# Performance work log

Hardware: AMD Instinct MI355X
Metric: run time of the kernel (lower is better)

Reference implementation:

```python
import jax, jax.numpy as jnp
import numpy as np

DIM = 1024
NEXP = 8
TOPK = 2
B, S = 2, 2048
HID = 4 * DIM

# ---- BitLinear (kyegomez/BitNet, 1.58-bit) helpers ----

def rmsnorm(x):
    # SimpleRMSNorm: x / rms(x), no learned scale
    return x * jax.lax.rsqrt(jnp.mean(x * x, axis=-1, keepdims=True) + 1e-6)

def act_quant(x):
    # per-token int8 absmax quant
    scale = 127.0 / jnp.clip(jnp.max(jnp.abs(x), axis=-1, keepdims=True), 1e-5, None)
    return jnp.clip(jnp.round(x * scale), -128, 127) / scale

def weight_quant(w):
    # ternary weight quant with per-tensor mean-abs scale
    scale = 1.0 / jnp.clip(jnp.mean(jnp.abs(w)), 1e-5, None)
    return jnp.clip(jnp.round(w * scale), -1, 1) / scale

def ste(a, q):
    # straight-through estimator: forward q, backward identity on a
    return a + jax.lax.stop_gradient(q - a)

def bit_input(x):
    xn = rmsnorm(x)
    return ste(xn, act_quant(xn))

def bit_weight(w):
    return ste(w, weight_quant(w))


def setup_inputs() -> dict:
    key = jax.random.key(0)
    ks = jax.random.split(key, 6)
    x = jax.random.normal(ks[0], (B, S, DIM), dtype=jnp.float32)
    eps = jax.random.normal(ks[1], (B, S, NEXP), dtype=jnp.float32)
    w_route = jax.random.normal(ks[2], (NEXP, DIM), dtype=jnp.float32) * 0.02
    w_noise = jax.random.normal(ks[3], (NEXP, DIM), dtype=jnp.float32) * 0.02
    w1 = jax.random.normal(ks[4], (NEXP, HID, DIM), dtype=jnp.float32) * 0.02
    w2 = jax.random.normal(ks[5], (NEXP, DIM, HID), dtype=jnp.float32) * 0.02
    return {"x": x, "eps": eps, "w_route": w_route, "w_noise": w_noise, "w1": w1, "w2": w2}


def reference(x, eps, w_route, w_noise, w1, w2):
    Bb, Ss, D = x.shape
    # router: both BitLinears share the same rmsnorm+quant of x (no bias)
    xq = bit_input(x)                                  # [B,S,D]
    logits = xq @ bit_weight(w_route).T                # [B,S,E]
    noise_logits = xq @ bit_weight(w_noise).T          # [B,S,E]
    noisy = logits + eps * jax.nn.softplus(noise_logits)
    _, topi = jax.lax.top_k(noisy, TOPK)               # indices [B,S,K]
    sel = jnp.any(jax.nn.one_hot(topi, NEXP, dtype=jnp.bool_), axis=-2)  # [B,S,E]
    sparse = jnp.where(sel, noisy, -jnp.inf)
    gates = jax.nn.softmax(sparse, axis=-1)            # zeros at unselected experts

    T = Bb * Ss
    xf = xq.reshape(T, D)                              # expert layer-1 input quant == router's
    gf = gates.reshape(T, NEXP)
    w1q = jax.vmap(bit_weight)(w1)                     # [E,H,D]
    w2q = jax.vmap(bit_weight)(w2)                     # [E,D,H]
    h = jax.nn.relu(jnp.einsum('td,ehd->teh', xf, w1q))
    hq = bit_input(h)                                  # per-(token,expert) quant
    y = jnp.einsum('teh,edh->ted', hq, w2q)            # expert outputs
    # gated combine; gates are exactly 0 for unselected experts -> identical to masked scatter-add
    out = jnp.einsum('ted,te->td', y, gf)
    return out.reshape(Bb, Ss, D)
```

## Files before the change

### kernel.cpp

```cpp
#include <hip/hip_runtime.h>
#include <hip/hip_bf16.h>

#define DIMD 1024
#define NEXP 8
#define NTOK 4096
#define HIDN 4096
#define CAP  4096
#define EXPSTRIDE 4194304L

typedef __bf16 bf16;
typedef bf16  bf16x8 __attribute__((ext_vector_type(8)));
typedef float f32x4  __attribute__((ext_vector_type(4)));
typedef int   i32x4  __attribute__((ext_vector_type(4)));
typedef signed char i8x8 __attribute__((ext_vector_type(8)));
typedef signed char i8x4 __attribute__((ext_vector_type(4)));
typedef signed char i8;

__device__ __forceinline__ void gload16(const void* g, void* l) {
  __builtin_amdgcn_global_load_lds(
      (const __attribute__((address_space(1))) unsigned int*)g,
      (__attribute__((address_space(3))) unsigned int*)l, 16, 0, 0);
}

#define VMCNT4 asm volatile("s_waitcnt vmcnt(4)" ::: "memory")
#define VMCNT0 asm volatile("s_waitcnt vmcnt(0)" ::: "memory")
#define BAR    asm volatile("s_barrier" ::: "memory")

__global__ void k_wsum(const float* __restrict__ w1, const float* __restrict__ w2,
                       float* __restrict__ partials) {
  const int slot = blockIdx.y;
  const int b = blockIdx.x;
  const int tid = threadIdx.x;
  const float* src = (slot < 8) ? (w1 + (long)slot * EXPSTRIDE)
                                : (w2 + (long)(slot - 8) * EXPSTRIDE);
  const f32x4* p = (const f32x4*)src;
  float s = 0.f;
  #pragma unroll
  for (int j = 0; j < 32; ++j) {
    f32x4 v = p[(long)b * 8192 + j * 256 + tid];
    s += fabsf(v.x) + fabsf(v.y) + fabsf(v.z) + fabsf(v.w);
  }
  #pragma unroll
  for (int o = 1; o < 64; o <<= 1) s += __shfl_xor(s, o, 64);
  __shared__ float red[4];
  if ((tid & 63) == 0) red[tid >> 6] = s;
  __syncthreads();
  if (tid == 0) partials[slot * 128 + b] = red[0] + red[1] + red[2] + red[3];
}

__global__ void k_finalize(const float* __restrict__ partials,
                           const float* __restrict__ wr, const float* __restrict__ wn,
                           float* __restrict__ wmean,
                           bf16* __restrict__ wrq, bf16* __restrict__ wnq) {
  const int tid = threadIdx.x;
  if (tid < 16) {
    float s = 0.f;
    for (int j = 0; j < 128; ++j) s += partials[tid * 128 + j];
    wmean[tid] = fmaxf(s * (1.0f / 4194304.0f), 1e-5f);
  }
  float sr = 0.f, sn = 0.f;
  #pragma unroll
  for (int j = 0; j < 32; ++j) {
    sr += fabsf(wr[j * 256 + tid]);
    sn += fabsf(wn[j * 256 + tid]);
  }
  #pragma unroll
  for (int o = 1; o < 64; o <<= 1) {
    sr += __shfl_xor(sr, o, 64);
    sn += __shfl_xor(sn, o, 64);
  }
  __shared__ float red[8];
  if ((tid & 63) == 0) { red[tid >> 6] = sr; red[4 + (tid >> 6)] = sn; }
  __syncthreads();
  if (tid == 0) {
    wmean[16] = fmaxf((red[0] + red[1] + red[2] + red[3]) * (1.0f / 8192.0f), 1e-5f);
    wmean[17] = fmaxf((red[4] + red[5] + red[6] + red[7]) * (1.0f / 8192.0f), 1e-5f);
  }
  __syncthreads();
  const float ir = 1.0f / wmean[16];
  const float in = 1.0f / wmean[17];
  for (int j = 0; j < 32; ++j) {
    int i = j * 256 + tid;
    wrq[i] = (bf16)fminf(fmaxf(rintf(wr[i] * ir), -1.f), 1.f);
    wnq[i] = (bf16)fminf(fmaxf(rintf(wn[i] * in), -1.f), 1.f);
  }
}

__global__ void k_wquant(const float* __restrict__ w1, const float* __restrict__ w2,
                         const float* __restrict__ wmean,
                         i8* __restrict__ w1q, i8* __restrict__ w2q) {
  const int tid = threadIdx.x;
  const int which = blockIdx.x >> 14;
  const long lg = (long)(blockIdx.x & 16383) * 256 + tid;
  const int e = (int)(lg >> 19);
  const float inv = 1.0f / wmean[(which ? 8 : 0) + e];
  const float* src = which ? w2 : w1;
  i8* dst = which ? w2q : w1q;
  const f32x4* p = (const f32x4*)src + lg * 2;
  f32x4 v0 = p[0], v1 = p[1];
  i8x8 q;
  q[0] = (i8)fminf(fmaxf(rintf(v0.x * inv), -1.f), 1.f);
  q[1] = (i8)fminf(fmaxf(rintf(v0.y * inv), -1.f), 1.f);
  q[2] = (i8)fminf(fmaxf(rintf(v0.z * inv), -1.f), 1.f);
  q[3] = (i8)fminf(fmaxf(rintf(v0.w * inv), -1.f), 1.f);
  q[4] = (i8)fminf(fmaxf(rintf(v1.x * inv), -1.f), 1.f);
  q[5] = (i8)fminf(fmaxf(rintf(v1.y * inv), -1.f), 1.f);
  q[6] = (i8)fminf(fmaxf(rintf(v1.z * inv), -1.f), 1.f);
  q[7] = (i8)fminf(fmaxf(rintf(v1.w * inv), -1.f), 1.f);
  *(i8x8*)(dst + lg * 8) = q;
}

__global__ void k_xquant(const float* __restrict__ x, i8* __restrict__ xq,
                         float* __restrict__ sx) {
  const int t = blockIdx.x, tid = threadIdx.x;
  f32x4 v = ((const f32x4*)(x + (long)t * DIMD))[tid];
  float ss = v.x * v.x + v.y * v.y + v.z * v.z + v.w * v.w;
  float am = fmaxf(fmaxf(fabsf(v.x), fabsf(v.y)), fmaxf(fabsf(v.z), fabsf(v.w)));
  #pragma unroll
  for (int o = 1; o < 64; o <<= 1) {
    ss += __shfl_xor(ss, o, 64);
    am = fmaxf(am, __shfl_xor(am, o, 64));
  }
  __shared__ float red[8];
  if ((tid & 63) == 0) { red[tid >> 6] = ss; red[4 + (tid >> 6)] = am; }
  __syncthreads();
  ss = red[0] + red[1] + red[2] + red[3];
  am = fmaxf(fmaxf(red[4], red[5]), fmaxf(red[6], red[7]));
  const float r = 1.0f / sqrtf(ss * (1.0f / DIMD) + 1e-6f);
  const float amn = fmaxf(am * r, 1e-5f);
  const float s = 127.0f / amn;
  i8x4 q;
  q[0] = (i8)fminf(fmaxf(rintf((v.x * r) * s), -128.f), 127.f);
  q[1] = (i8)fminf(fmaxf(rintf((v.y * r) * s), -128.f), 127.f);
  q[2] = (i8)fminf(fmaxf(rintf((v.z * r) * s), -128.f), 127.f);
  q[3] = (i8)fminf(fmaxf(rintf((v.w * r) * s), -128.f), 127.f);
  *(i8x4*)(xq + (long)t * DIMD + tid * 4) = q;
  if (tid == 0) sx[t] = amn * (1.0f / 127.0f);
}

__global__ void k_router(const i8* __restrict__ xq, const float* __restrict__ sx,
                         const bf16* __restrict__ wrq, const bf16* __restrict__ wnq,
                         const float* __restrict__ eps, const float* __restrict__ wmean,
                         int* __restrict__ cnt, int* __restrict__ idx,
                         float* __restrict__ gate) {
  __shared__ float xf[DIMD];
  __shared__ float dots[16];
  const int t = blockIdx.x, tid = threadIdx.x;
  const i8* xr = xq + (long)t * DIMD;
  #pragma unroll
  for (int j = 0; j < 4; ++j) xf[tid * 4 + j] = (float)xr[tid * 4 + j];
  __syncthreads();
  const int grp = tid >> 4, l16 = tid & 15;
  const bf16* wv = (grp < 8) ? (wrq + grp * DIMD) : (wnq + (grp - 8) * DIMD);
  float s = 0.f;
  #pragma unroll
  for (int j = 0; j < 64; ++j) s += xf[l16 + j * 16] * (float)wv[l16 + j * 16];
  s += __shfl_xor(s, 1, 64); s += __shfl_xor(s, 2, 64);
  s += __shfl_xor(s, 4, 64); s += __shfl_xor(s, 8, 64);
  if (l16 == 0) dots[grp] = s;
  __syncthreads();
  if (tid == 0) {
    const float st = sx[t];
    const float fr = st * wmean[16], fn = st * wmean[17];
    float ny[8];
    #pragma unroll
    for (int e = 0; e < 8; ++e) {
      const float nl = dots[8 + e] * fn;
      const float sp = fmaxf(nl, 0.f) + log1pf(expf(-fabsf(nl)));
      ny[e] = dots[e] * fr + eps[t * 8 + e] * sp;
    }
    int i1 = 0;
    #pragma unroll
    for (int e = 1; e < 8; ++e) if (ny[e] > ny[i1]) i1 = e;
    int i2 = (i1 == 0) ? 1 : 0;
    #pragma unroll
    for (int e = 0; e < 8; ++e) if (e != i1 && ny[e] > ny[i2]) i2 = e;
    const float ex = expf(ny[i2] - ny[i1]);
    const float g1 = 1.0f / (1.0f + ex);
    const float g2 = ex * g1;
    int p1 = atomicAdd(&cnt[i1], 1);
    idx[i1 * CAP + p1] = t; gate[i1 * CAP + p1] = g1;
    int p2 = atomicAdd(&cnt[i2], 1);
    idx[i2 * CAP + p2] = t; gate[i2 * CAP + p2] = g2;
  }
}

__global__ void k_offsets(const int* __restrict__ cnt, int* __restrict__ offs) {
  if (threadIdx.x == 0) {
    int a = 0;
    for (int e = 0; e < NEXP; ++e) { offs[e] = a; a += cnt[e]; }
    offs[8] = a;
  }
}

template <int KD, int LOGNT, bool L1>
__global__ __launch_bounds__(256, 4) void k_gemm(
    const i8* __restrict__ Abase, const i8* __restrict__ Wq,
    const int* __restrict__ cnt, const int* __restrict__ offs,
    const int* __restrict__ idx, const float* __restrict__ gate,
    const float* __restrict__ srow, const float* __restrict__ wmean,
    float* __restrict__ Out) {
  const int bid = blockIdx.x;
  const int xcd = bid & 7;
  const int s = bid >> 3;
  const int pl = s >> 5;
  const int mt = s & 31;
  const int pidx = pl * 8 + xcd;
  const int e = pidx >> LOGNT;
  const int nt = pidx & ((1 << LOGNT) - 1);

  const int c = cnt[e];
  if (mt * 128 >= c) return;
  const int oe = offs[e];
  __shared__ __align__(16) char lds[33280];
  char* lA0 = lds;
  char* lB0 = lds + 8192;
  char* lA1 = lds + 16384;
  char* lB1 = lds + 24576;
  int* tokL = (int*)(lds + 32768);
  const int tid = threadIdx.x, w = tid >> 6, lam = tid & 63;
  if (tid < 128) {
    int i = mt * 128 + tid;
    tokL[tid] = idx[e * CAP + (i < c ? i : c - 1)];
  }
  __syncthreads();

  const i8* aS[2];
  const i8* bS[2];
  #pragma unroll
  for (int i = 0; i < 2; ++i) {
    const int cid = w * 64 + lam + 256 * i;
    const int r = cid >> 2, q = cid & 3;
    const int cg = q ^ ((r >> 1) & 3);
    long arow;
    if (L1) arow = (long)tokL[r];
    else { int ii = mt * 128 + r; arow = (long)oe + (ii < c ? ii : c - 1); }
    aS[i] = Abase + arow * KD + cg * 16;
    bS[i] = Wq + (long)e * EXPSTRIDE + (long)(nt * 128 + r) * KD + cg * 16;
  }
  const int dbase = (w * 64 + lam) * 16;

  auto STAGE = [&](int kb, char* dA, char* dB) {
    #pragma unroll
    for (int i = 0; i < 2; ++i) gload16(aS[i] + kb * 64, dA + dbase + i * 4096);
    #pragma unroll
    for (int i = 0; i < 2; ++i) gload16(bS[i] + kb * 64, dB + dbase + i * 4096);
  };

  const int wr = w >> 1, wc = w & 1;
  int offA[4], offB[4];
  const int cc = lam >> 4;
  #pragma unroll
  for (int m = 0; m < 4; ++m) {
    const int ra = wr * 64 + m * 16 + (lam & 15);
    const int rb = wc * 64 + m * 16 + (lam & 15);
    offA[m] = ra * 64 + ((cc ^ ((ra >> 1) & 3)) << 4);
    offB[m] = rb * 64 + ((cc ^ ((rb >> 1) & 3)) << 4);
  }
  i32x4 acc[4][4];
  #pragma unroll
  for (int m = 0; m < 4; ++m)
    #pragma unroll
    for (int n = 0; n < 4; ++n) acc[m][n] = (i32x4){0, 0, 0, 0};

  auto COMPUTE = [&](const char* cA, const char* cB) {
    i32x4 af[4], bfr[4];
    #pragma unroll
    for (int m = 0; m < 4; ++m) af[m] = *(const i32x4*)(cA + offA[m]);
    #pragma unroll
    for (int n = 0; n < 4; ++n) bfr[n] = *(const i32x4*)(cB + offB[n]);
    #pragma unroll
    for (int m = 0; m < 4; ++m)
      #pragma unroll
      for (int n = 0; n < 4; ++n)
        acc[m][n] = __builtin_amdgcn_mfma_i32_16x16x64_i8(af[m], bfr[n], acc[m][n], 0, 0, 0);
  };

  constexpr int KT = KD / 64;
  STAGE(0, lA0, lB0);
  for (int kb = 0; kb < KT; kb += 2) {
    STAGE(kb + 1, lA1, lB1);
    VMCNT4;
    BAR;
    COMPUTE(lA0, lB0);
    BAR;
    if (kb + 2 < KT) { STAGE(kb + 2, lA0, lB0); VMCNT4; } else { VMCNT0; }
    BAR;
    COMPUTE(lA1, lB1);
    BAR;
  }

  const float wm = wmean[(L1 ? 0 : 8) + e];
  #pragma unroll
  for (int m = 0; m < 4; ++m) {
    #pragma unroll
    for (int r = 0; r < 4; ++r) {
      const int rl = wr * 64 + m * 16 + ((lam >> 4) << 2) + r;
      const int i = mt * 128 + rl;
      if (i < c) {
        if (L1) {
          const float fac = srow[tokL[rl]] * wm;
          float* hp = Out + (long)(oe + i) * HIDN + nt * 128 + wc * 64 + (lam & 15);
          #pragma unroll
          for (int n = 0; n < 4; ++n) hp[n * 16] = fmaxf((float)acc[m][n][r] * fac, 0.f);
        } else {
          const float fac = srow[oe + i] * wm * gate[e * CAP + i];
          float* op = Out + (long)tokL[rl] * DIMD + nt * 128 + wc * 64 + (lam & 15);
          #pragma unroll
          for (int n = 0; n < 4; ++n) atomicAdd(op + n * 16, (float)acc[m][n][r] * fac);
        }
      }
    }
  }
}

__global__ void k_hquant(const float* __restrict__ h, i8* __restrict__ hq,
                         float* __restrict__ sh, const int* __restrict__ offs) {
  const int row = blockIdx.x;
  if (row >= offs[8]) return;
  const int tid = threadIdx.x;
  const f32x4* hr = (const f32x4*)(h + (long)row * HIDN);
  f32x4 v[4];
  float ss = 0.f, am = 0.f;
  #pragma unroll
  for (int j = 0; j < 4; ++j) {
    v[j] = hr[tid + j * 256];
    ss += v[j].x * v[j].x + v[j].y * v[j].y + v[j].z * v[j].z + v[j].w * v[j].w;
    am = fmaxf(am, fmaxf(fmaxf(fabsf(v[j].x), fabsf(v[j].y)),
                         fmaxf(fabsf(v[j].z), fabsf(v[j].w))));
  }
  #pragma unroll
  for (int o = 1; o < 64; o <<= 1) {
    ss += __shfl_xor(ss, o, 64);
    am = fmaxf(am, __shfl_xor(am, o, 64));
  }
  __shared__ float red[8];
  if ((tid & 63) == 0) { red[tid >> 6] = ss; red[4 + (tid >> 6)] = am; }
  __syncthreads();
  ss = red[0] + red[1] + red[2] + red[3];
  am = fmaxf(fmaxf(red[4], red[5]), fmaxf(red[6], red[7]));
  const float r = 1.0f / sqrtf(ss * (1.0f / HIDN) + 1e-6f);
  const float amn = fmaxf(am * r, 1e-5f);
  const float s = 127.0f / amn;
  i8* dst = hq + (long)row * HIDN;
  #pragma unroll
  for (int j = 0; j < 4; ++j) {
    i8x4 q;
    q[0] = (i8)fminf(fmaxf(rintf((v[j].x * r) * s), -128.f), 127.f);
    q[1] = (i8)fminf(fmaxf(rintf((v[j].y * r) * s), -128.f), 127.f);
    q[2] = (i8)fminf(fmaxf(rintf((v[j].z * r) * s), -128.f), 127.f);
    q[3] = (i8)fminf(fmaxf(rintf((v[j].w * r) * s), -128.f), 127.f);
    *(i8x4*)(dst + (tid + j * 256) * 4) = q;
  }
  if (tid == 0) sh[row] = amn * (1.0f / 127.0f);
}

extern "C" void kernel_launch(void* const* d_in, const int* in_sizes, int n_in,
                              void* d_out, int out_size, void* d_ws, size_t ws_size,
                              hipStream_t stream) {
  const float* x   = (const float*)d_in[0];
  const float* eps = (const float*)d_in[1];
  const float* wr  = (const float*)d_in[2];
  const float* wn  = (const float*)d_in[3];
  const float* w1  = (const float*)d_in[4];
  const float* w2  = (const float*)d_in[5];
  float* out = (float*)d_out;
  (void)in_sizes; (void)n_in; (void)ws_size;

  char* ws = (char*)d_ws;
  size_t off = 0;
  auto alloc = [&](size_t bytes) -> void* {
    void* p = ws + off;
    off = (off + bytes + 255) & ~(size_t)255;
    return p;
  };
  i8*    w1q      = (i8*)alloc(33554432);
  i8*    w2q      = (i8*)alloc(33554432);
  bf16*  wrq      = (bf16*)alloc(16384);
  bf16*  wnq      = (bf16*)alloc(16384);
  i8*    xq       = (i8*)alloc(4194304);
  float* sx       = (float*)alloc(16384);
  float* sh       = (float*)alloc(32768);
  int*   idxb     = (int*)alloc(131072);
  float* gateb    = (float*)alloc(131072);
  int*   cntb     = (int*)alloc(64);
  int*   offsb    = (int*)alloc(64);
  float* partials = (float*)alloc(8192);
  float* wmean    = (float*)alloc(128);
  float* h        = (float*)alloc(134217728);
  i8*    hq       = (i8*)alloc(33554432);

  (void)hipMemsetAsync(out, 0, (size_t)out_size * sizeof(float), stream);
  (void)hipMemsetAsync(cntb, 0, 64, stream);

  k_wsum<<<dim3(128, 16), 256, 0, stream>>>(w1, w2, partials);
  k_finalize<<<1, 256, 0, stream>>>(partials, wr, wn, wmean, wrq, wnq);
  k_wquant<<<32768, 256, 0, stream>>>(w1, w2, wmean, w1q, w2q);
  k_xquant<<<NTOK, 256, 0, stream>>>(x, xq, sx);
  k_router<<<NTOK, 256, 0, stream>>>(xq, sx, wrq, wnq, eps, wmean, cntb, idxb, gateb);
  k_offsets<<<1, 64, 0, stream>>>(cntb, offsb);
  k_gemm<1024, 5, true><<<8192, 256, 0, stream>>>(
      xq, w1q, cntb, offsb, idxb, gateb, sx, wmean, h);
  k_hquant<<<8192, 256, 0, stream>>>(h, hq, sh, offsb);
  k_gemm<4096, 3, false><<<2048, 256, 0, stream>>>(
      hq, w2q, cntb, offsb, idxb, gateb, sh, wmean, out);
}
```

Baseline: 661.3 us.

## Use four-stage LDS pipeline for second expert GEMM

For the layer-2 GEMM (K=4096), the double-buffered loop becomes a 4-buffer ring that keeps three tiles of global loads in flight, with matching vmcnt waits. LDS use per block grows to about 64KB and launch bounds drop to 2 blocks per SM for that instantiation. The aim is to hide global load latency on the long-K GEMM, at the cost of fewer resident blocks. The layer-1 path is unchanged.

```diff
diff --git a/kernel.cpp b/kernel.cpp
--- a/kernel.cpp
+++ b/kernel.cpp
@@ -22,8 +22,10 @@
       (__attribute__((address_space(3))) unsigned int*)l, 16, 0, 0);
 }
 
-#define VMCNT4 asm volatile("s_waitcnt vmcnt(4)" ::: "memory")
-#define VMCNT0 asm volatile("s_waitcnt vmcnt(0)" ::: "memory")
+#define VMCNT12 asm volatile("s_waitcnt vmcnt(12)" ::: "memory")
+#define VMCNT8  asm volatile("s_waitcnt vmcnt(8)" ::: "memory")
+#define VMCNT4  asm volatile("s_waitcnt vmcnt(4)" ::: "memory")
+#define VMCNT0  asm volatile("s_waitcnt vmcnt(0)" ::: "memory")
 #define BAR    asm volatile("s_barrier" ::: "memory")
 
 __global__ void k_wsum(const float* __restrict__ w1, const float* __restrict__ w2,
@@ -194,7 +196,7 @@
 }
 
 template <int KD, int LOGNT, bool L1>
-__global__ __launch_bounds__(256, 4) void k_gemm(
+__global__ __launch_bounds__(256, L1 ? 4 : 2) void k_gemm(
     const i8* __restrict__ Abase, const i8* __restrict__ Wq,
     const int* __restrict__ cnt, const int* __restrict__ offs,
     const int* __restrict__ idx, const float* __restrict__ gate,
@@ -212,12 +214,9 @@
   const int c = cnt[e];
   if (mt * 128 >= c) return;
   const int oe = offs[e];
-  __shared__ __align__(16) char lds[33280];
-  char* lA0 = lds;
-  char* lB0 = lds + 8192;
-  char* lA1 = lds + 16384;
-  char* lB1 = lds + 24576;
-  int* tokL = (int*)(lds + 32768);
+  constexpr int NBUF = L1 ? 2 : 4;
+  __shared__ __align__(16) char lds[NBUF * 16384 + 512];
+  int* tokL = (int*)(lds + NBUF * 16384);
   const int tid = threadIdx.x, w = tid >> 6, lam = tid & 63;
   if (tid < 128) {
     int i = mt * 128 + tid;
@@ -277,17 +276,44 @@
   };
 
   constexpr int KT = KD / 64;
-  STAGE(0, lA0, lB0);
-  for (int kb = 0; kb < KT; kb += 2) {
-    STAGE(kb + 1, lA1, lB1);
-    VMCNT4;
-    BAR;
-    COMPUTE(lA0, lB0);
-    BAR;
-    if (kb + 2 < KT) { STAGE(kb + 2, lA0, lB0); VMCNT4; } else { VMCNT0; }
-    BAR;
-    COMPUTE(lA1, lB1);
-    BAR;
+  if constexpr (L1) {
+    char* lA0 = lds;            char* lB0 = lds + 8192;
+    char* lA1 = lds + 16384;    char* lB1 = lds + 24576;
+    STAGE(0, lA0, lB0);
+    for (int kb = 0; kb < KT; kb += 2) {
+      STAGE(kb + 1, lA1, lB1);
+      VMCNT4;
+      BAR;
+      COMPUTE(lA0, lB0);
+      BAR;
+      if (kb + 2 < KT) { STAGE(kb + 2, lA0, lB0); VMCNT4; } else { VMCNT0; }
+      BAR;
+      COMPUTE(lA1, lB1);
+      BAR;
+    }
+  } else {
+    char* bA[4]; char* bB[4];
+    #pragma unroll
+    for (int i = 0; i < 4; ++i) { bA[i] = lds + i * 16384; bB[i] = lds + i * 16384 + 8192; }
+    STAGE(0, bA[0], bB[0]);
+    STAGE(1, bA[1], bB[1]);
+    STAGE(2, bA[2], bB[2]);
+    int kb = 0;
+    for (; kb + 4 < KT; kb += 4) {
+      #pragma unroll
+      for (int p = 0; p < 4; ++p) {
+        STAGE(kb + 3 + p, bA[(p + 3) & 3], bB[(p + 3) & 3]);
+        VMCNT12;
+        BAR;
+        COMPUTE(bA[p], bB[p]);
+        BAR;
+      }
+    }
+    STAGE(KT - 1, bA[3], bB[3]);
+    VMCNT12; BAR; COMPUTE(bA[0], bB[0]); BAR;
+    VMCNT8;  BAR; COMPUTE(bA[1], bB[1]); BAR;
+    VMCNT4;  BAR; COMPUTE(bA[2], bB[2]); BAR;
+    VMCNT0;  BAR; COMPUTE(bA[3], bB[3]);
   }
 
   const float wm = wmean[(L1 ? 0 : 8) + e];
```

Measured after the change: 650.6 us. Within noise of the previous version (-1.6%).
